# Optimization experiments

Hardware: AMD Instinct MI355X
Metric: run time of the kernel (lower is better)

Reference implementation:

```python
import jax, jax.numpy as jnp
import numpy as np

VOCAB = 50000
DIM = 768


def setup_inputs() -> dict:
    key = jax.random.key(0)
    k1, k2, k3, k4 = jax.random.split(key, 4)
    token = jax.random.randint(k1, (32, 512), 0, VOCAB, dtype=jnp.int64)
    need_mapper = jax.random.randint(k2, (VOCAB,), 0, 2, dtype=jnp.int32)
    bert_embedding = jax.random.normal(k3, (VOCAB, DIM), dtype=jnp.float32)
    mapper_w = jax.random.normal(k4, (DIM, DIM), dtype=jnp.float32) * (1.0 / np.sqrt(DIM))
    mapper_b = jnp.zeros((DIM,), dtype=jnp.float32)
    return {
        "token": token,
        "need_mapper": need_mapper,
        "bert_embedding": bert_embedding,
        "mapper_w": mapper_w,
        "mapper_b": mapper_b,
    }


def reference(token, need_mapper, bert_embedding, mapper_w, mapper_b):
    # Gather: [B, S, D] -- irregular access into the embedding table.
    vecs = bert_embedding[token]
    # Conditional mapper (vectorized over all tokens; selected by per-id mask).
    mapped = jnp.einsum("bsd,de->bse", vecs, mapper_w) + mapper_b
    need = need_mapper[token].astype(bool)  # [B, S]
    return jnp.where(need[..., None], mapped, vecs)
```

## Files before the change

### kernel.cpp

```cpp
#include <hip/hip_runtime.h>
#include <hip/hip_bf16.h>
#include <stdint.h>
#include <stddef.h>

#define DIM 768

typedef short short8 __attribute__((ext_vector_type(8)));
typedef float f32x4 __attribute__((ext_vector_type(4)));

__device__ inline unsigned short f2bf_rne(float f) {
    union { float f; unsigned u; } x; x.f = f;
    unsigned r = x.u + 0x7fffu + ((x.u >> 16) & 1u);
    return (unsigned short)(r >> 16);
}

__device__ inline void gload_lds16(const void* g, void* l) {
    __builtin_amdgcn_global_load_lds((const __attribute__((address_space(1))) void*)g,
                                     (__attribute__((address_space(3))) void*)l, 16, 0, 0);
}

__global__ __launch_bounds__(256) void convw_kernel(
    const float* __restrict__ w, unsigned short* __restrict__ Bt)
{
    __shared__ unsigned short t[64][65];
    const int k0 = blockIdx.x * 64, n0 = blockIdx.y * 64;
    const int tid = threadIdx.x;
#pragma unroll
    for (int p = 0; p < 16; ++p) {
        int e = p * 256 + tid;
        int r = e >> 6, c = e & 63;
        t[c][r] = f2bf_rne(w[(size_t)(k0 + r) * DIM + n0 + c]);
    }
    __syncthreads();
#pragma unroll
    for (int p = 0; p < 16; ++p) {
        int e = p * 256 + tid;
        int r = e >> 6, c = e & 63;
        Bt[(size_t)(n0 + r) * DIM + k0 + c] = t[r][c];
    }
}

__global__ __launch_bounds__(256) void fused_gemm_kernel(
    const int* __restrict__ token,
    const int* __restrict__ need_mapper,
    const float* __restrict__ emb,
    const unsigned short* __restrict__ Bt,
    const float* __restrict__ bias,
    float* __restrict__ out)
{
    __shared__ float As[128 * 32];
    __shared__ unsigned short Bs[128 * 32];
    __shared__ int tok_s[128];
    __shared__ int flag_s[128];

    const int tid  = threadIdx.x;
    const int wave = tid >> 6;
    const int lane = tid & 63;
    const int quad = lane >> 4;
    const int l15  = lane & 15;
    const int wm   = wave >> 1;
    const int wn   = wave & 1;
    const int tile_m = blockIdx.x;
    const int tile_n = blockIdx.y;

    if (tid < 128) {
        int t = token[tile_m * 128 + tid];
        tok_s[tid]  = t;
        flag_s[tid] = need_mapper[t];
    }
    __syncthreads();

    const int r8 = tid >> 3;
    const int c8 = tid & 7;
    const float* pA[4];
#pragma unroll
    for (int j = 0; j < 4; ++j) {
        int r = j * 32 + r8;
        pA[j] = emb + (size_t)tok_s[r] * DIM + ((c8 ^ (r & 7)) << 2);
    }
    float* lA0 = As + (wave * 8) * 32;
    const unsigned short* pB = Bt + (size_t)(tile_n * 128 + (tid >> 2)) * DIM + (tid & 3) * 8;
    unsigned short* lB = Bs + wave * 512;

    f32x4 acc[4][4] = {};

    for (int kk = 0; kk < DIM; kk += 32) {
        __syncthreads();
#pragma unroll
        for (int j = 0; j < 4; ++j)
            gload_lds16(pA[j] + kk, lA0 + j * 32 * 32);
        gload_lds16(pB + kk,                   lB);
        gload_lds16(pB + kk + (size_t)64 * DIM, lB + 2048);
        __syncthreads();

        short8 af[4], bf[4];
#pragma unroll
        for (int i = 0; i < 4; ++i) {
            const int m = wm * 64 + i * 16 + l15;
            const float* row = As + (m << 5);
            f32x4 a0 = *(const f32x4*)(row + ((((quad << 1)    ) ^ (m & 7)) << 2));
            f32x4 a1 = *(const f32x4*)(row + ((((quad << 1) + 1) ^ (m & 7)) << 2));
            unsigned u0 = __float_as_uint(a0[0]) + 0x8000u;
            unsigned u1 = __float_as_uint(a0[1]) + 0x8000u;
            unsigned u2 = __float_as_uint(a0[2]) + 0x8000u;
            unsigned u3 = __float_as_uint(a0[3]) + 0x8000u;
            unsigned u4 = __float_as_uint(a1[0]) + 0x8000u;
            unsigned u5 = __float_as_uint(a1[1]) + 0x8000u;
            unsigned u6 = __float_as_uint(a1[2]) + 0x8000u;
            unsigned u7 = __float_as_uint(a1[3]) + 0x8000u;
            union { int i4[4]; short8 s; } pk;
            pk.i4[0] = __builtin_amdgcn_perm(u1, u0, 0x07060302);
            pk.i4[1] = __builtin_amdgcn_perm(u3, u2, 0x07060302);
            pk.i4[2] = __builtin_amdgcn_perm(u5, u4, 0x07060302);
            pk.i4[3] = __builtin_amdgcn_perm(u7, u6, 0x07060302);
            af[i] = pk.s;
        }
#pragma unroll
        for (int j = 0; j < 4; ++j)
            bf[j] = *(const short8*)(Bs + (wn * 64 + j * 16 + l15) * 32 + quad * 8);
#pragma unroll
        for (int i = 0; i < 4; ++i)
#pragma unroll
            for (int j = 0; j < 4; ++j)
                acc[i][j] = __builtin_amdgcn_mfma_f32_16x16x32_bf16(af[i], bf[j], acc[i][j], 0, 0, 0);
    }

    const int colg = tile_n * 128 + wn * 64 + l15;
    float bv[4];
#pragma unroll
    for (int j = 0; j < 4; ++j) bv[j] = bias[colg + j * 16];

#pragma unroll
    for (int i = 0; i < 4; ++i) {
#pragma unroll
        for (int r = 0; r < 4; ++r) {
            const int lrow = wm * 64 + i * 16 + quad * 4 + r;
            const int gm   = tile_m * 128 + lrow;
            float* orow = out + (size_t)gm * DIM + colg;
            if (flag_s[lrow]) {
#pragma unroll
                for (int j = 0; j < 4; ++j)
                    orow[j * 16] = acc[i][j][r] + bv[j];
            } else {
                const float* erow = emb + (size_t)tok_s[lrow] * DIM + colg;
#pragma unroll
                for (int j = 0; j < 4; ++j)
                    orow[j * 16] = erow[j * 16];
            }
        }
    }
}

extern "C" void kernel_launch(void* const* d_in, const int* in_sizes, int n_in,
                              void* d_out, int out_size, void* d_ws, size_t ws_size,
                              hipStream_t stream)
{
    const int*   token       = (const int*)d_in[0];
    const int*   need_mapper = (const int*)d_in[1];
    const float* emb         = (const float*)d_in[2];
    const float* w           = (const float*)d_in[3];
    const float* bias        = (const float*)d_in[4];
    float* out = (float*)d_out;

    const int ntok = in_sizes[0];

    unsigned short* Bt = (unsigned short*)d_ws;

    convw_kernel<<<dim3(DIM / 64, DIM / 64), dim3(256), 0, stream>>>(w, Bt);
    fused_gemm_kernel<<<dim3(ntok / 128, DIM / 128), dim3(256), 0, stream>>>(
        token, need_mapper, emb, Bt, bias, out);
}
```

Before: 241.7 us.

## Compact mapped tokens into bf16 buffer and run GEMM only on them

A new gather kernel copies unmapped rows straight to the output and compacts the mapped rows into a bf16 buffer, using an atomic counter and a per-slot index list. The GEMM then runs only over the compacted rows, with blocks beyond the count exiting early, and double-buffers its LDS tiles so the next K slice loads while the current one computes. This targets the roughly half of GEMM work spent on tokens whose result is discarded. It adds an extra kernel launch, a round trip through the bf16 intermediate buffer, scattered output writes, and output row order that depends on atomic timing.

```diff
diff --git a/kernel.cpp b/kernel.cpp
--- a/kernel.cpp
+++ b/kernel.cpp
@@ -1,5 +1,4 @@
 #include <hip/hip_runtime.h>
-#include <hip/hip_bf16.h>
 #include <stdint.h>
 #include <stddef.h>
 
@@ -7,6 +6,7 @@
 
 typedef short short8 __attribute__((ext_vector_type(8)));
 typedef float f32x4 __attribute__((ext_vector_type(4)));
+typedef unsigned short ushortx4 __attribute__((ext_vector_type(4)));
 
 __device__ inline unsigned short f2bf_rne(float f) {
     union { float f; unsigned u; } x; x.f = f;
@@ -20,8 +20,9 @@
 }
 
 __global__ __launch_bounds__(256) void convw_kernel(
-    const float* __restrict__ w, unsigned short* __restrict__ Bt)
-{
+    const float* __restrict__ w, unsigned short* __restrict__ Bt, int* __restrict__ counter)
+{
+    if (blockIdx.x == 0 && blockIdx.y == 0 && threadIdx.x == 0) *counter = 0;
     __shared__ unsigned short t[64][65];
     const int k0 = blockIdx.x * 64, n0 = blockIdx.y * 64;
     const int tid = threadIdx.x;
@@ -40,18 +41,78 @@
     }
 }
 
-__global__ __launch_bounds__(256) void fused_gemm_kernel(
+__global__ __launch_bounds__(256) void gather_kernel(
     const int* __restrict__ token,
     const int* __restrict__ need_mapper,
     const float* __restrict__ emb,
+    unsigned short* __restrict__ Ac,
+    int* __restrict__ idx,
+    int* __restrict__ counter,
+    float* __restrict__ out)
+{
+    __shared__ int tok_s[32];
+    __shared__ int slot_s[32];
+    const int tid = threadIdx.x;
+    const int base = blockIdx.x * 32;
+
+    if (tid < 64) {
+        int t = 0, nm = 0;
+        if (tid < 32) { t = token[base + tid]; nm = need_mapper[t]; }
+        unsigned long long m = __ballot(nm != 0);
+        int bb = 0;
+        if (tid == 0) { int c = __popcll(m); if (c) bb = atomicAdd(counter, c); }
+        bb = __shfl(bb, 0);
+        if (tid < 32) {
+            tok_s[tid] = t;
+            int s = -1;
+            if (nm) {
+                s = bb + __popcll(m & ((1ull << tid) - 1ull));
+                idx[s] = base + tid;
+            }
+            slot_s[tid] = s;
+        }
+    }
+    __syncthreads();
+
+    const int wave = tid >> 6, lane = tid & 63;
+    for (int tk = wave; tk < 32; tk += 4) {
+        const float* src = emb + (size_t)tok_s[tk] * DIM;
+        const int slot = slot_s[tk];
+        if (slot < 0) {
+            float* dst = out + (size_t)(base + tk) * DIM;
+#pragma unroll
+            for (int p = 0; p < 3; ++p)
+                *(f32x4*)(dst + p * 256 + lane * 4) = *(const f32x4*)(src + p * 256 + lane * 4);
+        } else {
+            unsigned short* dst = Ac + (size_t)slot * DIM;
+#pragma unroll
+            for (int p = 0; p < 3; ++p) {
+                f32x4 v = *(const f32x4*)(src + p * 256 + lane * 4);
+                ushortx4 h;
+                h[0] = f2bf_rne(v[0]); h[1] = f2bf_rne(v[1]);
+                h[2] = f2bf_rne(v[2]); h[3] = f2bf_rne(v[3]);
+                *(ushortx4*)(dst + p * 256 + lane * 4) = h;
+            }
+        }
+    }
+}
+
+__global__ __launch_bounds__(256) void gemm_kernel(
+    const unsigned short* __restrict__ Ac,
     const unsigned short* __restrict__ Bt,
+    const int* __restrict__ idx,
+    const int* __restrict__ counter,
     const float* __restrict__ bias,
     float* __restrict__ out)
 {
-    __shared__ float As[128 * 32];
-    __shared__ unsigned short Bs[128 * 32];
-    __shared__ int tok_s[128];
-    __shared__ int flag_s[128];
+    const int count = *counter;
+    const int tile_m = blockIdx.x;
+    if (tile_m * 128 >= count) return;
+    const int tile_n = blockIdx.y;
+
+    __shared__ unsigned short As[2][128 * 32];
+    __shared__ unsigned short Bs[2][128 * 32];
+    __shared__ int idx_s[128];
 
     const int tid  = threadIdx.x;
     const int wave = tid >> 6;
@@ -60,70 +121,56 @@
     const int l15  = lane & 15;
     const int wm   = wave >> 1;
     const int wn   = wave & 1;
-    const int tile_m = blockIdx.x;
-    const int tile_n = blockIdx.y;
 
     if (tid < 128) {
-        int t = token[tile_m * 128 + tid];
-        tok_s[tid]  = t;
-        flag_s[tid] = need_mapper[t];
-    }
+        int s = tile_m * 128 + tid;
+        idx_s[tid] = (s < count) ? idx[s] : 0;
+    }
+
+    const int ra = tid >> 2, sa = tid & 3;
+    const unsigned short* pA0 = Ac + (size_t)(tile_m * 128 + ra) * DIM + ((sa ^ ((ra >> 1) & 3)) << 3);
+    const unsigned short* pA1 = Ac + (size_t)(tile_m * 128 + 64 + ra) * DIM + ((sa ^ (((64 + ra) >> 1) & 3)) << 3);
+    const unsigned short* pB0 = Bt + (size_t)(tile_n * 128 + ra) * DIM + ((sa ^ ((ra >> 1) & 3)) << 3);
+    const unsigned short* pB1 = Bt + (size_t)(tile_n * 128 + 64 + ra) * DIM + ((sa ^ (((64 + ra) >> 1) & 3)) << 3);
+
+#define STAGE(b, kk) do { \
+    gload_lds16(pA0 + (kk), &As[(b)][wave * 512]); \
+    gload_lds16(pA1 + (kk), &As[(b)][2048 + wave * 512]); \
+    gload_lds16(pB0 + (kk), &Bs[(b)][wave * 512]); \
+    gload_lds16(pB1 + (kk), &Bs[(b)][2048 + wave * 512]); \
+} while (0)
+
+    f32x4 acc[4][4] = {};
+
+#define COMPUTE(b) do { \
+    short8 af[4], bf[4]; \
+    _Pragma("unroll") \
+    for (int i = 0; i < 4; ++i) { \
+        int m = wm * 64 + i * 16 + l15; \
+        af[i] = *(const short8*)(&As[(b)][m * 32 + ((quad ^ ((m >> 1) & 3)) << 3)]); \
+    } \
+    _Pragma("unroll") \
+    for (int j = 0; j < 4; ++j) { \
+        int n = wn * 64 + j * 16 + l15; \
+        bf[j] = *(const short8*)(&Bs[(b)][n * 32 + ((quad ^ ((n >> 1) & 3)) << 3)]); \
+    } \
+    _Pragma("unroll") \
+    for (int i = 0; i < 4; ++i) \
+        _Pragma("unroll") \
+        for (int j = 0; j < 4; ++j) \
+            acc[i][j] = __builtin_amdgcn_mfma_f32_16x16x32_bf16(af[i], bf[j], acc[i][j], 0, 0, 0); \
+} while (0)
+
+    STAGE(0, 0);
     __syncthreads();
-
-    const int r8 = tid >> 3;
-    const int c8 = tid & 7;
-    const float* pA[4];
-#pragma unroll
-    for (int j = 0; j < 4; ++j) {
-        int r = j * 32 + r8;
-        pA[j] = emb + (size_t)tok_s[r] * DIM + ((c8 ^ (r & 7)) << 2);
-    }
-    float* lA0 = As + (wave * 8) * 32;
-    const unsigned short* pB = Bt + (size_t)(tile_n * 128 + (tid >> 2)) * DIM + (tid & 3) * 8;
-    unsigned short* lB = Bs + wave * 512;
-
-    f32x4 acc[4][4] = {};
-
-    for (int kk = 0; kk < DIM; kk += 32) {
+    int cur = 0;
+    for (int kk = 32; kk < DIM; kk += 32) {
+        STAGE(cur ^ 1, kk);
+        COMPUTE(cur);
         __syncthreads();
-#pragma unroll
-        for (int j = 0; j < 4; ++j)
-            gload_lds16(pA[j] + kk, lA0 + j * 32 * 32);
-        gload_lds16(pB + kk,                   lB);
-        gload_lds16(pB + kk + (size_t)64 * DIM, lB + 2048);
-        __syncthreads();
-
-        short8 af[4], bf[4];
-#pragma unroll
-        for (int i = 0; i < 4; ++i) {
-            const int m = wm * 64 + i * 16 + l15;
-            const float* row = As + (m << 5);
-            f32x4 a0 = *(const f32x4*)(row + ((((quad << 1)    ) ^ (m & 7)) << 2));
-            f32x4 a1 = *(const f32x4*)(row + ((((quad << 1) + 1) ^ (m & 7)) << 2));
-            unsigned u0 = __float_as_uint(a0[0]) + 0x8000u;
-            unsigned u1 = __float_as_uint(a0[1]) + 0x8000u;
-            unsigned u2 = __float_as_uint(a0[2]) + 0x8000u;
-            unsigned u3 = __float_as_uint(a0[3]) + 0x8000u;
-            unsigned u4 = __float_as_uint(a1[0]) + 0x8000u;
-            unsigned u5 = __float_as_uint(a1[1]) + 0x8000u;
-            unsigned u6 = __float_as_uint(a1[2]) + 0x8000u;
-            unsigned u7 = __float_as_uint(a1[3]) + 0x8000u;
-            union { int i4[4]; short8 s; } pk;
-            pk.i4[0] = __builtin_amdgcn_perm(u1, u0, 0x07060302);
-            pk.i4[1] = __builtin_amdgcn_perm(u3, u2, 0x07060302);
-            pk.i4[2] = __builtin_amdgcn_perm(u5, u4, 0x07060302);
-            pk.i4[3] = __builtin_amdgcn_perm(u7, u6, 0x07060302);
-            af[i] = pk.s;
-        }
-#pragma unroll
-        for (int j = 0; j < 4; ++j)
-            bf[j] = *(const short8*)(Bs + (wn * 64 + j * 16 + l15) * 32 + quad * 8);
-#pragma unroll
-        for (int i = 0; i < 4; ++i)
-#pragma unroll
-            for (int j = 0; j < 4; ++j)
-                acc[i][j] = __builtin_amdgcn_mfma_f32_16x16x32_bf16(af[i], bf[j], acc[i][j], 0, 0, 0);
-    }
+        cur ^= 1;
+    }
+    COMPUTE(cur);
 
     const int colg = tile_n * 128 + wn * 64 + l15;
     float bv[4];
@@ -135,20 +182,17 @@
 #pragma unroll
         for (int r = 0; r < 4; ++r) {
             const int lrow = wm * 64 + i * 16 + quad * 4 + r;
-            const int gm   = tile_m * 128 + lrow;
-            float* orow = out + (size_t)gm * DIM + colg;
-            if (flag_s[lrow]) {
+            const int slot = tile_m * 128 + lrow;
+            if (slot < count) {
+                float* orow = out + (size_t)idx_s[lrow] * DIM + colg;
 #pragma unroll
                 for (int j = 0; j < 4; ++j)
                     orow[j * 16] = acc[i][j][r] + bv[j];
-            } else {
-                const float* erow = emb + (size_t)tok_s[lrow] * DIM + colg;
-#pragma unroll
-                for (int j = 0; j < 4; ++j)
-                    orow[j * 16] = erow[j * 16];
             }
         }
     }
+#undef STAGE
+#undef COMPUTE
 }
 
 extern "C" void kernel_launch(void* const* d_in, const int* in_sizes, int n_in,
@@ -165,8 +209,13 @@
     const int ntok = in_sizes[0];
 
     unsigned short* Bt = (unsigned short*)d_ws;
-
-    convw_kernel<<<dim3(DIM / 64, DIM / 64), dim3(256), 0, stream>>>(w, Bt);
-    fused_gemm_kernel<<<dim3(ntok / 128, DIM / 128), dim3(256), 0, stream>>>(
-        token, need_mapper, emb, Bt, bias, out);
-}
+    unsigned short* Ac = (unsigned short*)((char*)d_ws + (1u << 21));
+    int* idx     = (int*)((char*)d_ws + (1u << 21) + (size_t)16384 * DIM * 2);
+    int* counter = idx + 16384;
+
+    convw_kernel<<<dim3(DIM / 64, DIM / 64), dim3(256), 0, stream>>>(w, Bt, counter);
+    gather_kernel<<<dim3(ntok / 32), dim3(256), 0, stream>>>(
+        token, need_mapper, emb, Ac, idx, counter, out);
+    gemm_kernel<<<dim3(ntok / 128, DIM / 128), dim3(256), 0, stream>>>(
+        Ac, Bt, idx, counter, bias, out);
+}
```

Result: slower. 253.2 us (+4.7%).

## Double-buffer LDS tiles, swizzle B layout, and remap blocks across XCDs

Applied to the files above, without the earlier changes.

Adds double-buffered LDS for the A and B tiles, so the global-to-LDS loads for the next K slice are issued before computing the current one, and drops one barrier per iteration. Applies an XOR swizzle to the B tile in LDS to reduce bank conflicts. Flattens the grid to 1D and remaps block IDs so that consecutive work groups on the same XCD share an M tile (all 6 N tiles), which improves L2 reuse of the gathered embedding rows. Doubling LDS use may lower occupancy.

```diff
diff --git a/kernel.cpp b/kernel.cpp
--- a/kernel.cpp
+++ b/kernel.cpp
@@ -1,5 +1,4 @@
 #include <hip/hip_runtime.h>
-#include <hip/hip_bf16.h>
 #include <stdint.h>
 #include <stddef.h>
 
@@ -48,8 +47,14 @@
     const float* __restrict__ bias,
     float* __restrict__ out)
 {
-    __shared__ float As[128 * 32];
-    __shared__ unsigned short Bs[128 * 32];
+    const int cpx  = gridDim.x >> 3;
+    const int orig = blockIdx.x;
+    const int wgid = (orig & 7) * cpx + (orig >> 3);
+    const int tile_m = wgid / 6;
+    const int tile_n = wgid - tile_m * 6;
+
+    __shared__ float          As[2][128 * 32];
+    __shared__ unsigned short Bs[2][128 * 32];
     __shared__ int tok_s[128];
     __shared__ int flag_s[128];
 
@@ -60,8 +65,6 @@
     const int l15  = lane & 15;
     const int wm   = wave >> 1;
     const int wn   = wave & 1;
-    const int tile_m = blockIdx.x;
-    const int tile_n = blockIdx.y;
 
     if (tid < 128) {
         int t = token[tile_m * 128 + tid];
@@ -78,52 +81,66 @@
         int r = j * 32 + r8;
         pA[j] = emb + (size_t)tok_s[r] * DIM + ((c8 ^ (r & 7)) << 2);
     }
-    float* lA0 = As + (wave * 8) * 32;
-    const unsigned short* pB = Bt + (size_t)(tile_n * 128 + (tid >> 2)) * DIM + (tid & 3) * 8;
-    unsigned short* lB = Bs + wave * 512;
+    const int rb = tid >> 2;
+    const int sb = tid & 3;
+    const unsigned short* pB0 = Bt + (size_t)(tile_n * 128 + rb) * DIM + ((sb ^ ((rb >> 1) & 3)) << 3);
+    const unsigned short* pB1 = Bt + (size_t)(tile_n * 128 + 64 + rb) * DIM + ((sb ^ (((64 + rb) >> 1) & 3)) << 3);
+
+#define STAGE(b, kk) do { \
+    _Pragma("unroll") \
+    for (int j = 0; j < 4; ++j) \
+        gload_lds16(pA[j] + (kk), &As[(b)][wave * 256 + j * 1024]); \
+    gload_lds16(pB0 + (kk), &Bs[(b)][wave * 512]); \
+    gload_lds16(pB1 + (kk), &Bs[(b)][2048 + wave * 512]); \
+} while (0)
 
     f32x4 acc[4][4] = {};
 
-    for (int kk = 0; kk < DIM; kk += 32) {
+#define COMPUTE(b) do { \
+    short8 af[4], bf[4]; \
+    _Pragma("unroll") \
+    for (int i = 0; i < 4; ++i) { \
+        const int m = wm * 64 + i * 16 + l15; \
+        const float* row = &As[(b)][m << 5]; \
+        f32x4 a0 = *(const f32x4*)(row + ((((quad << 1)    ) ^ (m & 7)) << 2)); \
+        f32x4 a1 = *(const f32x4*)(row + ((((quad << 1) + 1) ^ (m & 7)) << 2)); \
+        unsigned u0 = __float_as_uint(a0[0]) + 0x8000u; \
+        unsigned u1 = __float_as_uint(a0[1]) + 0x8000u; \
+        unsigned u2 = __float_as_uint(a0[2]) + 0x8000u; \
+        unsigned u3 = __float_as_uint(a0[3]) + 0x8000u; \
+        unsigned u4 = __float_as_uint(a1[0]) + 0x8000u; \
+        unsigned u5 = __float_as_uint(a1[1]) + 0x8000u; \
+        unsigned u6 = __float_as_uint(a1[2]) + 0x8000u; \
+        unsigned u7 = __float_as_uint(a1[3]) + 0x8000u; \
+        union { int i4[4]; short8 s; } pk; \
+        pk.i4[0] = __builtin_amdgcn_perm(u1, u0, 0x07060302); \
+        pk.i4[1] = __builtin_amdgcn_perm(u3, u2, 0x07060302); \
+        pk.i4[2] = __builtin_amdgcn_perm(u5, u4, 0x07060302); \
+        pk.i4[3] = __builtin_amdgcn_perm(u7, u6, 0x07060302); \
+        af[i] = pk.s; \
+    } \
+    _Pragma("unroll") \
+    for (int j = 0; j < 4; ++j) { \
+        const int n = wn * 64 + j * 16 + l15; \
+        bf[j] = *(const short8*)(&Bs[(b)][n * 32 + ((quad ^ ((n >> 1) & 3)) << 3)]); \
+    } \
+    _Pragma("unroll") \
+    for (int i = 0; i < 4; ++i) \
+        _Pragma("unroll") \
+        for (int j = 0; j < 4; ++j) \
+            acc[i][j] = __builtin_amdgcn_mfma_f32_16x16x32_bf16(af[i], bf[j], acc[i][j], 0, 0, 0); \
+} while (0)
+
+    STAGE(0, 0);
+    __syncthreads();
+    int cur = 0;
+    for (int kk = 32; kk < DIM; kk += 32) {
+        STAGE(cur ^ 1, kk);
+        COMPUTE(cur);
         __syncthreads();
-#pragma unroll
-        for (int j = 0; j < 4; ++j)
-            gload_lds16(pA[j] + kk, lA0 + j * 32 * 32);
-        gload_lds16(pB + kk,                   lB);
-        gload_lds16(pB + kk + (size_t)64 * DIM, lB + 2048);
-        __syncthreads();
-
-        short8 af[4], bf[4];
-#pragma unroll
-        for (int i = 0; i < 4; ++i) {
-            const int m = wm * 64 + i * 16 + l15;
-            const float* row = As + (m << 5);
-            f32x4 a0 = *(const f32x4*)(row + ((((quad << 1)    ) ^ (m & 7)) << 2));
-            f32x4 a1 = *(const f32x4*)(row + ((((quad << 1) + 1) ^ (m & 7)) << 2));
-            unsigned u0 = __float_as_uint(a0[0]) + 0x8000u;
-            unsigned u1 = __float_as_uint(a0[1]) + 0x8000u;
-            unsigned u2 = __float_as_uint(a0[2]) + 0x8000u;
-            unsigned u3 = __float_as_uint(a0[3]) + 0x8000u;
-            unsigned u4 = __float_as_uint(a1[0]) + 0x8000u;
-            unsigned u5 = __float_as_uint(a1[1]) + 0x8000u;
-            unsigned u6 = __float_as_uint(a1[2]) + 0x8000u;
-            unsigned u7 = __float_as_uint(a1[3]) + 0x8000u;
-            union { int i4[4]; short8 s; } pk;
-            pk.i4[0] = __builtin_amdgcn_perm(u1, u0, 0x07060302);
-            pk.i4[1] = __builtin_amdgcn_perm(u3, u2, 0x07060302);
-            pk.i4[2] = __builtin_amdgcn_perm(u5, u4, 0x07060302);
-            pk.i4[3] = __builtin_amdgcn_perm(u7, u6, 0x07060302);
-            af[i] = pk.s;
-        }
-#pragma unroll
-        for (int j = 0; j < 4; ++j)
-            bf[j] = *(const short8*)(Bs + (wn * 64 + j * 16 + l15) * 32 + quad * 8);
-#pragma unroll
-        for (int i = 0; i < 4; ++i)
-#pragma unroll
-            for (int j = 0; j < 4; ++j)
-                acc[i][j] = __builtin_amdgcn_mfma_f32_16x16x32_bf16(af[i], bf[j], acc[i][j], 0, 0, 0);
+        cur ^= 1;
     }
+    COMPUTE(cur);
 
     const int colg = tile_n * 128 + wn * 64 + l15;
     float bv[4];
@@ -149,6 +166,8 @@
             }
         }
     }
+#undef STAGE
+#undef COMPUTE
 }
 
 extern "C" void kernel_launch(void* const* d_in, const int* in_sizes, int n_in,
@@ -167,6 +186,6 @@
     unsigned short* Bt = (unsigned short*)d_ws;
 
     convw_kernel<<<dim3(DIM / 64, DIM / 64), dim3(256), 0, stream>>>(w, Bt);
-    fused_gemm_kernel<<<dim3(ntok / 128, DIM / 128), dim3(256), 0, stream>>>(
+    fused_gemm_kernel<<<dim3((ntok / 128) * 6), dim3(256), 0, stream>>>(
         token, need_mapper, emb, Bt, bias, out);
 }
```

Result: slower. 285.7 us (+18.2%).
